# Kernel optimization log

Hardware: AMD Instinct MI355X
Metric: run time of the kernel (lower is better)

The kernel has to match this reference:

```python
import jax, jax.numpy as jnp
import numpy as np
from jax import lax

B, CO, CI, KH, KW, H, W = 32, 128, 128, 3, 3, 56, 56
STRIDE = (1, 1)
PADDING = ((1, 1), (1, 1))


def setup_inputs() -> dict:
    key = jax.random.key(0)
    k1, k2, k3, k4 = jax.random.split(key, 4)
    inp = jax.random.normal(k1, (B, CI, H, W), dtype=jnp.float32)
    eps = jax.random.normal(k2, (B, CO, CI, KH, KW), dtype=jnp.float32)
    # reset_parameters: psi ~ U(-6, -5); mu ~ U(-stdv, stdv), stdv = 1/sqrt(CI*KH*KW)
    weight_psi = jax.random.uniform(k3, (CO, CI, KH, KW), dtype=jnp.float32,
                                    minval=-6.0, maxval=-5.0)
    stdv = 1.0 / np.sqrt(CI * KH * KW)
    weight_mu = jax.random.uniform(k4, (CO, CI, KH, KW), dtype=jnp.float32,
                                   minval=-stdv, maxval=stdv)
    return {"input": inp, "eps": eps, "weight_psi": weight_psi, "weight_mu": weight_mu}


def reference(input, eps, weight_psi, weight_mu):
    # mul_exp_add: per-sample weight = eps * exp(psi) + mu  -> [B, CO, CI, KH, KW]
    weight = eps * jnp.exp(weight_psi) + weight_mu

    # Per-example conv (torch does it via groups = bs trick); here vmap over batch.
    def conv_one(x, w):  # x: [CI,H,W], w: [CO,CI,KH,KW]
        return lax.conv_general_dilated(
            x[None], w, window_strides=STRIDE, padding=PADDING,
            dimension_numbers=("NCHW", "OIHW", "NCHW"))[0]

    out = jax.vmap(conv_one)(input, weight)  # [B, CO, H, W]
    return out
```

## Files before the change

kernel.cpp:

```cpp
#include <hip/hip_runtime.h>
#include <hip/hip_bf16.h>

#define CO    128
#define CI    128
#define NPIX  3136
#define PH    58
#define PPIX  3364
#define HPX   232
#define SROW  272

typedef __bf16 bf16x8 __attribute__((ext_vector_type(8)));
typedef float  f32x4  __attribute__((ext_vector_type(4)));

__global__ void prep_all(const float* __restrict__ in,
                         const float* __restrict__ eps,
                         const float* __restrict__ psi,
                         const float* __restrict__ mu,
                         __bf16* __restrict__ wt,
                         __bf16* __restrict__ it) {
  __shared__ __align__(16) __bf16 T[64][136];
  const int bx = blockIdx.x, tid = threadIdx.x;

  if (bx < 2048) {
    int idx = bx * 256 + tid;
    int ci = idx & 127;
    int co = (idx >> 7) & 127;
    const float* e  = eps + (size_t)idx * 9;
    const float* ps = psi + (size_t)(co * CI + ci) * 9;
    const float* m  = mu  + (size_t)(co * CI + ci) * 9;
    float v[9];
#pragma unroll
    for (int p = 0; p < 9; ++p) v[p] = e[p] * __expf(ps[p]) + m[p];
    int b = idx >> 14;
    __bf16* w = wt + ((size_t)b * 9 * CO + co) * CI + ci;
#pragma unroll
    for (int p = 0; p < 9; ++p) w[(size_t)p * CO * CI] = (__bf16)v[p];
  } else if (bx < 2504) {
    int cid = (bx - 2048) * 256 + tid;
    int pid = cid >> 4;
    int chunk = cid & 15;
    int b = pid / 228;
    int e = pid - b * 228;
    int ph, pw;
    if (e < 58)       { ph = 0;       pw = e; }
    else if (e < 116) { ph = 57;      pw = e - 58; }
    else if (e < 172) { ph = e - 115; pw = 0; }
    else              { ph = e - 171; pw = 57; }
    f32x4 z = {0.f, 0.f, 0.f, 0.f};
    *(f32x4*)&it[((size_t)b * PPIX + ph * PH + pw) * CI + chunk * 8] = z;
  } else {
    int tx = bx - 2504;
    int b  = tx / 49;
    int p0 = (tx - b * 49) * 64;
    const float* src = in + (size_t)b * CI * NPIX;
#pragma unroll
    for (int jj = 0; jj < 8; ++jj) {
      int c = jj * 256 + tid;
      int ci = c >> 4, xc = c & 15;
      float4 v = *(const float4*)(src + (size_t)ci * NPIX + p0 + xc * 4);
      T[xc * 4 + 0][ci] = (__bf16)v.x;
      T[xc * 4 + 1][ci] = (__bf16)v.y;
      T[xc * 4 + 2][ci] = (__bf16)v.z;
      T[xc * 4 + 3][ci] = (__bf16)v.w;
    }
    __syncthreads();
    __bf16* dstb = it + (size_t)b * PPIX * CI;
#pragma unroll
    for (int jj = 0; jj < 4; ++jj) {
      int c = jj * 256 + tid;
      int pl = c >> 4, xc = c & 15;
      int pix = p0 + pl;
      int oh = pix / 56, ow = pix - oh * 56;
      int ppix = (oh + 1) * PH + (ow + 1);
      *(f32x4*)&dstb[(size_t)ppix * CI + xc * 8] = *(const f32x4*)&T[pl][xc * 8];
    }
  }
}

__global__ __launch_bounds__(256) void bconv_gemm(
    const __bf16* __restrict__ wt,
    const __bf16* __restrict__ it,
    float* __restrict__ out) {
  __shared__ __align__(16) char Bsh[HPX * SROW];
  const int tid  = threadIdx.x;
  const int w    = tid >> 6;
  const int lane = tid & 63;
  const int quad = lane >> 4;
  const int l15  = lane & 15;

  const int lin = blockIdx.x;
  const int x   = lin & 7;
  const int j   = lin >> 3;
  const int bhi = j & 3;
  const int tile = j >> 2;
  const int b   = x + 8 * bhi;
  const int oh0 = tile * 2;

  const __bf16* hsrc = it + ((size_t)b * PPIX + oh0 * PH) * CI;
#pragma unroll
  for (int i = 0; i < 15; ++i) {
    int idx = i * 256 + tid;
    if (idx < HPX * 16) {
      int px = idx >> 4, sub = idx & 15;
      f32x4 v = *(const f32x4*)(hsrc + (size_t)idx * 8);
      *(f32x4*)&Bsh[px * SROW + sub * 16] = v;
    }
  }
  __syncthreads();

  int bbase[7];
#pragma unroll
  for (int nf = 0; nf < 7; ++nf) {
    int n = nf * 16 + l15;
    int r = (n >= 56) ? 1 : 0;
    int c = n - r * 56;
    bbase[nf] = (r * PH + c) * SROW + quad * 16;
  }

  const int co0 = w * 32;
  const __bf16* wtb = wt + (size_t)b * 9 * CO * CI;
  const int ab0 = (co0 +      l15) * CI + quad * 8;
  const int ab1 = (co0 + 16 + l15) * CI + quad * 8;

  f32x4 acc[2][7] = {};
  bf16x8 acur[2], anxt[2];
  acur[0] = *(const bf16x8*)(wtb + ab0);
  acur[1] = *(const bf16x8*)(wtb + ab1);

#pragma unroll
  for (int s = 0; s < 36; ++s) {
    const int p   = s >> 2;
    const int ci0 = (s & 3) << 5;
    if (s < 35) {
      const int pn   = (s + 1) >> 2;
      const int ci0n = ((s + 1) & 3) << 5;
      const __bf16* ap = wtb + pn * (CO * CI) + ci0n;
      anxt[0] = *(const bf16x8*)(ap + ab0);
      anxt[1] = *(const bf16x8*)(ap + ab1);
    }
    const int kh = p / 3, kw = p - kh * 3;
    const int tapb = (kh * PH + kw) * SROW + ci0 * 2;
#pragma unroll
    for (int nf = 0; nf < 7; ++nf) {
      bf16x8 bfr = *(const bf16x8*)&Bsh[bbase[nf] + tapb];
      acc[0][nf] = __builtin_amdgcn_mfma_f32_16x16x32_bf16(acur[0], bfr, acc[0][nf], 0, 0, 0);
      acc[1][nf] = __builtin_amdgcn_mfma_f32_16x16x32_bf16(acur[1], bfr, acc[1][nf], 0, 0, 0);
    }
    acur[0] = anxt[0];
    acur[1] = anxt[1];
  }

  float* ob = out + (size_t)b * CO * NPIX + oh0 * 56;
#pragma unroll
  for (int mf = 0; mf < 2; ++mf) {
#pragma unroll
    for (int nf = 0; nf < 7; ++nf) {
#pragma unroll
      for (int r = 0; r < 4; ++r) {
        int co = co0 + mf * 16 + quad * 4 + r;
        ob[(size_t)co * NPIX + nf * 16 + l15] = acc[mf][nf][r];
      }
    }
  }
}

extern "C" void kernel_launch(void* const* d_in, const int* in_sizes, int n_in,
                              void* d_out, int out_size, void* d_ws, size_t ws_size,
                              hipStream_t stream) {
  const float* inp = (const float*)d_in[0];
  const float* eps = (const float*)d_in[1];
  const float* psi = (const float*)d_in[2];
  const float* mu  = (const float*)d_in[3];

  __bf16* wt = (__bf16*)d_ws;
  __bf16* it = (__bf16*)((char*)d_ws + 9437184);

  prep_all<<<4072, 256, 0, stream>>>(inp, eps, psi, mu, wt, it);
  bconv_gemm<<<896, 256, 0, stream>>>(wt, it, (float*)d_out);
}
```

Measured before the change: 159.6 us.

## Split GEMM warps over output channels and reduction halves with LDS reduction

```diff
diff --git a/kernel.cpp b/kernel.cpp
--- a/kernel.cpp
+++ b/kernel.cpp
@@ -87,6 +87,8 @@
   const int lane = tid & 63;
   const int quad = lane >> 4;
   const int l15  = lane & 15;
+  const int cg   = w & 1;
+  const int kg   = w >> 1;
 
   const int lin = blockIdx.x;
   const int x   = lin & 7;
@@ -114,51 +116,70 @@
     int n = nf * 16 + l15;
     int r = (n >= 56) ? 1 : 0;
     int c = n - r * 56;
-    bbase[nf] = (r * PH + c) * SROW + quad * 16;
-  }
-
-  const int co0 = w * 32;
-  const __bf16* wtb = wt + (size_t)b * 9 * CO * CI;
-  const int ab0 = (co0 +      l15) * CI + quad * 8;
-  const int ab1 = (co0 + 16 + l15) * CI + quad * 8;
-
-  f32x4 acc[2][7] = {};
-  bf16x8 acur[2], anxt[2];
-  acur[0] = *(const bf16x8*)(wtb + ab0);
-  acur[1] = *(const bf16x8*)(wtb + ab1);
-
-#pragma unroll
-  for (int s = 0; s < 36; ++s) {
-    const int p   = s >> 2;
-    const int ci0 = (s & 3) << 5;
-    if (s < 35) {
-      const int pn   = (s + 1) >> 2;
-      const int ci0n = ((s + 1) & 3) << 5;
-      const __bf16* ap = wtb + pn * (CO * CI) + ci0n;
-      anxt[0] = *(const bf16x8*)(ap + ab0);
-      anxt[1] = *(const bf16x8*)(ap + ab1);
-    }
+    bbase[nf] = (r * PH + c) * SROW + quad * 16 + kg * 128;
+  }
+
+  const int co0 = cg * 64;
+  const __bf16* wtb = wt + (size_t)b * 9 * CO * CI + kg * 64;
+  int ab[4];
+#pragma unroll
+  for (int mf = 0; mf < 4; ++mf)
+    ab[mf] = (co0 + mf * 16 + l15) * CI + quad * 8;
+
+  f32x4 acc[4][7] = {};
+  bf16x8 areg[3][4];
+#pragma unroll
+  for (int mf = 0; mf < 4; ++mf) areg[0][mf] = *(const bf16x8*)(wtb + ab[mf]);
+#pragma unroll
+  for (int mf = 0; mf < 4; ++mf) areg[1][mf] = *(const bf16x8*)(wtb + 32 + ab[mf]);
+
+#pragma unroll
+  for (int s = 0; s < 18; ++s) {
+    if (s < 16) {
+      const int p2  = (s + 2) >> 1;
+      const int kk2 = (s + 2) & 1;
+      const __bf16* ap = wtb + p2 * (CO * CI) + kk2 * 32;
+#pragma unroll
+      for (int mf = 0; mf < 4; ++mf)
+        areg[(s + 2) % 3][mf] = *(const bf16x8*)(ap + ab[mf]);
+    }
+    const int p  = s >> 1;
+    const int kk = s & 1;
     const int kh = p / 3, kw = p - kh * 3;
-    const int tapb = (kh * PH + kw) * SROW + ci0 * 2;
+    const int tapb = (kh * PH + kw) * SROW + kk * 64;
 #pragma unroll
     for (int nf = 0; nf < 7; ++nf) {
       bf16x8 bfr = *(const bf16x8*)&Bsh[bbase[nf] + tapb];
-      acc[0][nf] = __builtin_amdgcn_mfma_f32_16x16x32_bf16(acur[0], bfr, acc[0][nf], 0, 0, 0);
-      acc[1][nf] = __builtin_amdgcn_mfma_f32_16x16x32_bf16(acur[1], bfr, acc[1][nf], 0, 0, 0);
-    }
-    acur[0] = anxt[0];
-    acur[1] = anxt[1];
-  }
-
-  float* ob = out + (size_t)b * CO * NPIX + oh0 * 56;
-#pragma unroll
-  for (int mf = 0; mf < 2; ++mf) {
-#pragma unroll
-    for (int nf = 0; nf < 7; ++nf) {
-#pragma unroll
-      for (int r = 0; r < 4; ++r) {
-        int co = co0 + mf * 16 + quad * 4 + r;
-        ob[(size_t)co * NPIX + nf * 16 + l15] = acc[mf][nf][r];
+#pragma unroll
+      for (int mf = 0; mf < 4; ++mf)
+        acc[mf][nf] = __builtin_amdgcn_mfma_f32_16x16x32_bf16(areg[s % 3][mf], bfr, acc[mf][nf], 0, 0, 0);
+    }
+  }
+
+  __syncthreads();
+  if (kg == 1) {
+    char* rb = Bsh + cg * 28672;
+#pragma unroll
+    for (int mf = 0; mf < 4; ++mf)
+#pragma unroll
+      for (int nf = 0; nf < 7; ++nf)
+        *(f32x4*)(rb + ((mf * 7 + nf) * 64 + lane) * 16) = acc[mf][nf];
+  }
+  __syncthreads();
+  if (kg == 0) {
+    char* rb = Bsh + cg * 28672;
+    float* ob = out + (size_t)b * CO * NPIX + oh0 * 56;
+#pragma unroll
+    for (int mf = 0; mf < 4; ++mf) {
+#pragma unroll
+      for (int nf = 0; nf < 7; ++nf) {
+        f32x4 part = *(const f32x4*)(rb + ((mf * 7 + nf) * 64 + lane) * 16);
+        f32x4 v = acc[mf][nf] + part;
+#pragma unroll
+        for (int r = 0; r < 4; ++r) {
+          int co = co0 + mf * 16 + quad * 4 + r;
+          ob[(size_t)co * NPIX + nf * 16 + l15] = v[r];
+        }
       }
     }
   }
```

Result: slower. 170.1 us (+6.6%).
